# Performance work log

Hardware: AMD Instinct MI355X
Metric: run time of the kernel (lower is better)

The kernel has to match this reference:

```python
import jax, jax.numpy as jnp
import numpy as np


def setup_inputs() -> dict:
    key = jax.random.key(0)
    ks = jax.random.split(key, 8)
    B, T, U = 4, 256, 128
    De, Dp, D, V = 512, 512, 640, 1024
    s = lambda k, sh, fan: jax.random.normal(k, sh, dtype=jnp.float32) / np.sqrt(fan)
    return {
        "enc": jax.random.normal(ks[0], (B, T, De), dtype=jnp.float32),
        "pred": jax.random.normal(ks[1], (B, U, Dp), dtype=jnp.float32),
        "W_enc": s(ks[2], (De, D), De),
        "b_enc": jnp.zeros((D,), jnp.float32),
        "W_pred": s(ks[3], (Dp, D), Dp),
        "b_pred": jnp.zeros((D,), jnp.float32),
        "W_joint": s(ks[4], (D, V), D),
        "b_joint": jnp.zeros((V,), jnp.float32),
    }


def reference(enc, pred, W_enc, b_enc, W_pred, b_pred, W_joint, b_joint):
    # f: [B,T,D], g: [B,U,D]
    f = jnp.einsum("bte,ed->btd", enc, W_enc) + b_enc
    g = jnp.einsum("bup,pd->bud", pred, W_pred) + b_pred
    # broadcast-add over the T x U lattice, tanh activation
    joint = jnp.tanh(f[:, :, None, :] + g[:, None, :, :])  # [B,T,U,D]
    # final projection to num_classes
    out = jnp.einsum("btud,dv->btuv", joint, W_joint) + b_joint  # [B,T,U,V]
    return out
```

## Files before the change

### kernel.cpp

```cpp
#include <hip/hip_runtime.h>
#include <hip/hip_bf16.h>
#include <stdint.h>

typedef unsigned short u16;
typedef __attribute__((ext_vector_type(8))) __bf16 bf16x8;
typedef __attribute__((ext_vector_type(4))) float f32x4;
typedef __attribute__((ext_vector_type(8))) unsigned short u16x8;
typedef __attribute__((ext_vector_type(4))) unsigned int u32x4;

static __device__ __forceinline__ u16 f2bf(float x) {
  __hip_bfloat16 h = __float2bfloat16(x);
  u16 u;
  __builtin_memcpy(&u, &h, 2);
  return u;
}

static __device__ __forceinline__ float fast_tanh(float x) {
  float e = __expf(2.0f * x);
  return 1.0f - 2.0f * __builtin_amdgcn_rcpf(e + 1.0f);
}

static __device__ __forceinline__ void gload_lds16(const void* g, void* l) {
  __builtin_amdgcn_global_load_lds(
      (const __attribute__((address_space(1))) unsigned int*)g,
      (__attribute__((address_space(3))) unsigned int*)l, 16, 0, 0);
}

static __device__ __forceinline__ int swz(int row, int byte_in_row) {
  return row * 128 + (byte_in_row ^ ((row & 7) << 4));
}

__global__ __launch_bounds__(256) void transpose_cast_kernel(
    const float* __restrict__ in, u16* __restrict__ out, int K, int N) {
  int n = blockIdx.x;
  for (int k = threadIdx.x; k < K; k += 256) {
    out[(size_t)n * K + k] = f2bf(in[(size_t)k * N + n]);
  }
}

__global__ __launch_bounds__(256) void linear_kernel(
    const float* __restrict__ A, const u16* __restrict__ Wt,
    const float* __restrict__ bias, float* __restrict__ out) {
  __shared__ u16 sA[64 * 64];
  __shared__ u16 sB[64 * 64];
  const int t = threadIdx.x;
  const int bx = blockIdx.x;
  const int m0 = (bx / 10) * 64;
  const int n0 = (bx % 10) * 64;
  const int lane = t & 63, wid = t >> 6;
  const int wr = wid >> 1, wc = wid & 1;
  const int l15 = lane & 15, lk8 = (lane >> 4) << 3;

  const int srow = t >> 2;
  const int kc = (t & 3) << 4;

  f32x4 acc[2][2] = {};

  for (int k0 = 0; k0 < 512; k0 += 64) {
    {
      const float4* gp = (const float4*)(A + (size_t)(m0 + srow) * 512 + k0 + kc);
      u16 tmp[16];
#pragma unroll
      for (int i = 0; i < 4; ++i) {
        float4 v = gp[i];
        tmp[i * 4 + 0] = f2bf(v.x);
        tmp[i * 4 + 1] = f2bf(v.y);
        tmp[i * 4 + 2] = f2bf(v.z);
        tmp[i * 4 + 3] = f2bf(v.w);
      }
      *(u16x8*)((char*)sA + swz(srow, kc * 2)) = *(u16x8*)&tmp[0];
      *(u16x8*)((char*)sA + swz(srow, kc * 2 + 16)) = *(u16x8*)&tmp[8];
    }
    {
      const int off = (t & 3) << 5;
      const char* gsrc = (const char*)Wt + ((size_t)(n0 + srow) * 512 + k0) * 2 + off;
      u32x4 q0 = *(const u32x4*)gsrc;
      u32x4 q1 = *(const u32x4*)(gsrc + 16);
      *(u32x4*)((char*)sB + swz(srow, off)) = q0;
      *(u32x4*)((char*)sB + swz(srow, off + 16)) = q1;
    }
    __syncthreads();
#pragma unroll
    for (int kh = 0; kh < 2; ++kh) {
      const int kbyte = kh * 64 + lk8 * 2;
      bf16x8 av[2], bv[2];
#pragma unroll
      for (int mf = 0; mf < 2; ++mf)
        av[mf] = *(const bf16x8*)((char*)sA + swz(wr * 32 + mf * 16 + l15, kbyte));
#pragma unroll
      for (int nf = 0; nf < 2; ++nf)
        bv[nf] = *(const bf16x8*)((char*)sB + swz(wc * 32 + nf * 16 + l15, kbyte));
#pragma unroll
      for (int mf = 0; mf < 2; ++mf)
#pragma unroll
        for (int nf = 0; nf < 2; ++nf)
          acc[mf][nf] = __builtin_amdgcn_mfma_f32_16x16x32_bf16(
              av[mf], bv[nf], acc[mf][nf], 0, 0, 0);
    }
    __syncthreads();
  }

  const int r4 = (lane >> 4) << 2;
#pragma unroll
  for (int nf = 0; nf < 2; ++nf) {
    const int nc = n0 + wc * 32 + nf * 16 + l15;
    const float bjv = bias[nc];
#pragma unroll
    for (int mf = 0; mf < 2; ++mf) {
      const int mr = m0 + wr * 32 + mf * 16 + r4;
#pragma unroll
      for (int r = 0; r < 4; ++r)
        out[(size_t)(mr + r) * 640 + nc] = acc[mf][nf][r] + bjv;
    }
  }
}

__global__ __launch_bounds__(256) void joint_kernel(
    const float* __restrict__ f, const float* __restrict__ g,
    u16* __restrict__ joint, int m_base) {
  int idx = blockIdx.x * 256 + threadIdx.x;
  int row = idx / 80;
  int kc = (idx % 80) * 8;
  int m = m_base + row;
  int bt = m >> 7;
  int b = bt >> 8;
  int u = m & 127;
  const float4* fp = (const float4*)(f + (size_t)bt * 640 + kc);
  const float4* gp = (const float4*)(g + ((size_t)(b * 128 + u)) * 640 + kc);
  u16 tmp[8];
#pragma unroll
  for (int i = 0; i < 2; ++i) {
    float4 fv = fp[i];
    float4 gv = gp[i];
    tmp[i * 4 + 0] = f2bf(fast_tanh(fv.x + gv.x));
    tmp[i * 4 + 1] = f2bf(fast_tanh(fv.y + gv.y));
    tmp[i * 4 + 2] = f2bf(fast_tanh(fv.z + gv.z));
    tmp[i * 4 + 3] = f2bf(fast_tanh(fv.w + gv.w));
  }
  *(u16x8*)(joint + (size_t)row * 640 + kc) = *(u16x8*)&tmp[0];
}

__global__ __launch_bounds__(512, 2) void gemm256_kernel(
    const u16* __restrict__ A,
    const u16* __restrict__ Bt,
    const float* __restrict__ bias,
    float* __restrict__ out,
    int m_base, int mtiles) {
  extern __shared__ char smem[];
  const int t = threadIdx.x;
  const int lane = t & 63, wid = t >> 6;

  const int nwg = mtiles * 4;
  const int bid = blockIdx.x;
  const int q = nwg >> 3, r = nwg & 7;
  const int xcd = bid & 7, local = bid >> 3;
  const int wgid = (xcd < r ? xcd * (q + 1) : r * (q + 1) + (xcd - r) * q) + local;
  const int mt = wgid >> 2, nt = wgid & 3;

  const int wr = wid >> 2, wc = wid & 3;
  const int l15 = lane & 15;
  const int colbyte = (((lane >> 4) ^ ((l15 >> 1) & 3)) << 4);

  const int srow = lane >> 2;
  const int scol = ((lane & 3) ^ ((lane >> 3) & 3)) << 3;
  const u16* aS = A + (size_t)(mt * 256 + wid * 16 + srow) * 640 + scol;
  const u16* bS = Bt + (size_t)(nt * 256 + wid * 16 + srow) * 640 + scol;
  const int ldsbase = wid * 1024;

#define STAGE(kt, slot)                                              \
  do {                                                               \
    const int ko_ = (kt) * 32;                                       \
    char* sb_ = smem + (slot) * 32768;                               \
    gload_lds16(aS + ko_, sb_ + ldsbase);                            \
    gload_lds16(aS + 128 * 640 + ko_, sb_ + 8192 + ldsbase);         \
    gload_lds16(bS + ko_, sb_ + 16384 + ldsbase);                    \
    gload_lds16(bS + 128 * 640 + ko_, sb_ + 24576 + ldsbase);        \
  } while (0)

  f32x4 acc[8][4] = {};

  STAGE(0, 0);
  STAGE(1, 1);
  STAGE(2, 2);

  for (int tt = 0; tt < 20; ++tt) {
    asm volatile("s_waitcnt vmcnt(8)" ::: "memory");
    __builtin_amdgcn_s_barrier();
    __builtin_amdgcn_sched_barrier(0);
    const int kt = (tt + 3 > 19) ? 19 : tt + 3;
    STAGE(kt, (tt + 3) & 3);

    const char* sA = smem + (tt & 3) * 32768;
    const char* sB = sA + 16384;
    bf16x8 av[8], bv[4];
#pragma unroll
    for (int nf = 0; nf < 4; ++nf)
      bv[nf] = *(const bf16x8*)(sB + (wc * 64 + nf * 16 + l15) * 64 + colbyte);
#pragma unroll
    for (int mi = 0; mi < 8; ++mi)
      av[mi] = *(const bf16x8*)(sA + (wr * 128 + mi * 16 + l15) * 64 + colbyte);

    __builtin_amdgcn_s_setprio(1);
#pragma unroll
    for (int mi = 0; mi < 8; ++mi)
#pragma unroll
      for (int nf = 0; nf < 4; ++nf)
        acc[mi][nf] = __builtin_amdgcn_mfma_f32_16x16x32_bf16(
            av[mi], bv[nf], acc[mi][nf], 0, 0, 0);
    __builtin_amdgcn_s_setprio(0);
    __builtin_amdgcn_sched_barrier(0);
  }
#undef STAGE

  const int r4 = (lane >> 4) << 2;
#pragma unroll
  for (int nf = 0; nf < 4; ++nf) {
    const int v = nt * 256 + wc * 64 + nf * 16 + l15;
    const float bjv = bias[v];
#pragma unroll
    for (int mf = 0; mf < 8; ++mf) {
      const size_t m = (size_t)m_base + (size_t)mt * 256 + wr * 128 + mf * 16 + r4;
#pragma unroll
      for (int rr = 0; rr < 4; ++rr)
        out[(m + rr) * 1024 + v] = acc[mf][nf][rr] + bjv;
    }
  }
}

__global__ __launch_bounds__(512) void fused_joint_kernel(
    const float* __restrict__ f, const float* __restrict__ g,
    const u16* __restrict__ Wjt, const float* __restrict__ bj,
    float* __restrict__ out) {
  __shared__ u16 sA[128 * 64];
  __shared__ u16 sB[256 * 64];
  const int t = threadIdx.x;
  const int bt = blockIdx.x;
  const int b = bt >> 8;
  const int v0 = blockIdx.y << 8;
  const float* frow = f + (size_t)bt * 640;
  const float* gbase = g + (size_t)b * 128 * 640;

  const int lane = t & 63, wid = t >> 6;
  const int wr = wid >> 2, wc = wid & 3;
  const int l15 = lane & 15, lk8 = (lane >> 4) << 3;

  const int au = t >> 2;
  const int akc = (t & 3) << 4;
  const int bn = t >> 1;
  const int boff = (t & 1) << 6;

  f32x4 acc[4][4] = {};

  for (int k0 = 0; k0 < 640; k0 += 64) {
    {
      const float4* gp = (const float4*)(gbase + (size_t)au * 640 + k0 + akc);
      const float4* fp = (const float4*)(frow + k0 + akc);
      u16 tmp[16];
#pragma unroll
      for (int i = 0; i < 4; ++i) {
        float4 gv = gp[i];
        float4 fv = fp[i];
        tmp[i * 4 + 0] = f2bf(fast_tanh(gv.x + fv.x));
        tmp[i * 4 + 1] = f2bf(fast_tanh(gv.y + fv.y));
        tmp[i * 4 + 2] = f2bf(fast_tanh(gv.z + fv.z));
        tmp[i * 4 + 3] = f2bf(fast_tanh(gv.w + fv.w));
      }
      *(u16x8*)((char*)sA + swz(au, akc * 2)) = *(u16x8*)&tmp[0];
      *(u16x8*)((char*)sA + swz(au, akc * 2 + 16)) = *(u16x8*)&tmp[8];
    }
    {
      const char* gsrc = (const char*)Wjt + ((size_t)(v0 + bn) * 640 + k0) * 2 + boff;
#pragma unroll
      for (int i = 0; i < 4; ++i) {
        u32x4 qv = *(const u32x4*)(gsrc + i * 16);
        *(u32x4*)((char*)sB + swz(bn, boff + i * 16)) = qv;
      }
    }
    __syncthreads();
#pragma unroll
    for (int kh = 0; kh < 2; ++kh) {
      const int kbyte = kh * 64 + lk8 * 2;
      bf16x8 av[4], bv[4];
#pragma unroll
      for (int mf = 0; mf < 4; ++mf)
        av[mf] = *(const bf16x8*)((char*)sA + swz(wr * 64 + mf * 16 + l15, kbyte));
#pragma unroll
      for (int nf = 0; nf < 4; ++nf)
        bv[nf] = *(const bf16x8*)((char*)sB + swz(wc * 64 + nf * 16 + l15, kbyte));
#pragma unroll
      for (int mf = 0; mf < 4; ++mf)
#pragma unroll
        for (int nf = 0; nf < 4; ++nf)
          acc[mf][nf] = __builtin_amdgcn_mfma_f32_16x16x32_bf16(
              av[mf], bv[nf], acc[mf][nf], 0, 0, 0);
    }
    __syncthreads();
  }

  const int r4 = (lane >> 4) << 2;
#pragma unroll
  for (int nf = 0; nf < 4; ++nf) {
    const int v = v0 + wc * 64 + nf * 16 + l15;
    const float bjv = bj[v];
#pragma unroll
    for (int mf = 0; mf < 4; ++mf) {
      const int u = wr * 64 + mf * 16 + r4;
      const size_t o = ((size_t)bt * 128 + u) * 1024 + v;
#pragma unroll
      for (int rr = 0; rr < 4; ++rr)
        out[o + (size_t)rr * 1024] = acc[mf][nf][rr] + bjv;
    }
  }
}

extern "C" void kernel_launch(void* const* d_in, const int* in_sizes, int n_in,
                              void* d_out, int out_size, void* d_ws, size_t ws_size,
                              hipStream_t stream) {
  const float* enc = (const float*)d_in[0];
  const float* pred = (const float*)d_in[1];
  const float* W_enc = (const float*)d_in[2];
  const float* b_enc = (const float*)d_in[3];
  const float* W_pred = (const float*)d_in[4];
  const float* b_pred = (const float*)d_in[5];
  const float* W_joint = (const float*)d_in[6];
  const float* b_joint = (const float*)d_in[7];
  float* out = (float*)d_out;

  char* ws = (char*)d_ws;
  float* f = (float*)ws;
  float* gbuf = (float*)(ws + 2621440);
  u16* Wet = (u16*)(ws + 2621440 + 1310720);
  u16* Wpt = (u16*)(ws + 2621440 + 1310720 + 655360);
  u16* Wjt = (u16*)(ws + 2621440 + 1310720 + 2 * 655360);
  const size_t fixed = 2621440 + 1310720 + 2 * 655360 + 1310720;
  u16* joint = (u16*)(ws + fixed);

  transpose_cast_kernel<<<640, 256, 0, stream>>>(W_enc, Wet, 512, 640);
  transpose_cast_kernel<<<640, 256, 0, stream>>>(W_pred, Wpt, 512, 640);
  transpose_cast_kernel<<<1024, 256, 0, stream>>>(W_joint, Wjt, 640, 1024);

  linear_kernel<<<16 * 10, 256, 0, stream>>>(enc, Wet, b_enc, f);
  linear_kernel<<<8 * 10, 256, 0, stream>>>(pred, Wpt, b_pred, gbuf);

  const long TOTAL_M = 131072;
  long maxrows = ws_size > fixed ? (long)((ws_size - fixed) / 1280) : 0;
  maxrows &= ~255L;

  if (maxrows >= 16384) {
    (void)hipFuncSetAttribute((const void*)gemm256_kernel,
                              hipFuncAttributeMaxDynamicSharedMemorySize, 131072);
    long CH = maxrows >= TOTAL_M ? TOTAL_M : maxrows;
    for (long m0 = 0; m0 < TOTAL_M; m0 += CH) {
      long R = TOTAL_M - m0 < CH ? TOTAL_M - m0 : CH;
      int mtiles = (int)(R / 256);
      joint_kernel<<<(int)(R / 128) * 40, 256, 0, stream>>>(f, gbuf, joint, (int)m0);
      gemm256_kernel<<<mtiles * 4, 512, 131072, stream>>>(joint, Wjt, b_joint, out,
                                                          (int)m0, mtiles);
    }
  } else {
    fused_joint_kernel<<<dim3(1024, 4), 512, 0, stream>>>(f, gbuf, Wjt, b_joint, out);
  }
}
```

Before: 367.5 us.

## Restructure GEMM mainloop to double-buffered K=64 tiles with interleaved staging

Replaces the 4-slot K=32 pipeline in the projection GEMM with a 2-slot double buffer of K=64 tiles (128-byte LDS rows with a new XOR swizzle). Each iteration is split into four quarter phases that interleave LDS reads, MFMA bursts and the next tile's global-to-LDS loads. Each phase is separated by barriers and lgkmcnt waits. This halves the loop trip count and aims to overlap memory traffic with compute more finely. The cost is more barriers per iteration and a shallower prefetch distance, which could expose global load latency.

```diff
diff --git a/kernel.cpp b/kernel.cpp
--- a/kernel.cpp
+++ b/kernel.cpp
@@ -159,58 +159,101 @@
 
   const int wr = wid >> 2, wc = wid & 3;
   const int l15 = lane & 15;
-  const int colbyte = (((lane >> 4) ^ ((l15 >> 1) & 3)) << 4);
-
-  const int srow = lane >> 2;
-  const int scol = ((lane & 3) ^ ((lane >> 3) & 3)) << 3;
-  const u16* aS = A + (size_t)(mt * 256 + wid * 16 + srow) * 640 + scol;
-  const u16* bS = Bt + (size_t)(nt * 256 + wid * 16 + srow) * 640 + scol;
-  const int ldsbase = wid * 1024;
-
-#define STAGE(kt, slot)                                              \
-  do {                                                               \
-    const int ko_ = (kt) * 32;                                       \
-    char* sb_ = smem + (slot) * 32768;                               \
-    gload_lds16(aS + ko_, sb_ + ldsbase);                            \
-    gload_lds16(aS + 128 * 640 + ko_, sb_ + 8192 + ldsbase);         \
-    gload_lds16(bS + ko_, sb_ + 16384 + ldsbase);                    \
-    gload_lds16(bS + 128 * 640 + ko_, sb_ + 24576 + ldsbase);        \
+  const int kb16 = (lane >> 4) << 4;
+  const int rx = (l15 & 7) << 4;
+
+  const int scol = (((lane & 7) ^ (lane >> 3)) << 3);
+  const size_t rowsel = (size_t)(wid * 8 + (lane >> 3)) * 640 + scol;
+  const u16* a0 = A + (size_t)(mt * 256) * 640 + rowsel;
+  const u16* a1 = a0 + (size_t)64 * 640;
+  const u16* a2p = a0 + (size_t)128 * 640;
+  const u16* a3 = a0 + (size_t)192 * 640;
+  const u16* b0 = Bt + (size_t)(nt * 256) * 640 + rowsel;
+  const u16* b1 = b0 + (size_t)64 * 640;
+  const u16* b2p = b0 + (size_t)128 * 640;
+  const u16* b3 = b0 + (size_t)192 * 640;
+  const int ldst = wid * 1024;
+
+#define STAGE_HALF(kt, h, nb)                                               \
+  do {                                                                      \
+    const int ko_ = (kt) * 64;                                              \
+    gload_lds16(((h) == 0 ? a0 : (h) == 1 ? a2p : (h) == 2 ? b0 : b2p) + ko_, \
+                smem + (nb) + (h) * 16384 + ldst);                          \
+    gload_lds16(((h) == 0 ? a1 : (h) == 1 ? a3 : (h) == 2 ? b1 : b3) + ko_, \
+                smem + (nb) + (h) * 16384 + 8192 + ldst);                   \
   } while (0)
 
+#define DSREAD_B(kkb)                                                       \
+  _Pragma("unroll") for (int nf = 0; nf < 4; ++nf) bv[nf] =                 \
+      *(const bf16x8*)(sB + (wc * 64 + nf * 16 + l15) * 128 +               \
+                       (((kkb) + kb16) ^ rx));
+
+#define DSREAD_A(mi0, kkb)                                                  \
+  _Pragma("unroll") for (int i = 0; i < 4; ++i) av[i] =                     \
+      *(const bf16x8*)(sA + (wr * 128 + ((mi0) + i) * 16 + l15) * 128 +     \
+                       (((kkb) + kb16) ^ rx));
+
+#define MFMA16(mi0)                                                         \
+  __builtin_amdgcn_s_setprio(1);                                            \
+  _Pragma("unroll") for (int i = 0; i < 4; ++i)                             \
+  _Pragma("unroll") for (int nf = 0; nf < 4; ++nf)                          \
+      acc[(mi0) + i][nf] = __builtin_amdgcn_mfma_f32_16x16x32_bf16(         \
+          av[i], bv[nf], acc[(mi0) + i][nf], 0, 0, 0);                      \
+  __builtin_amdgcn_s_setprio(0);
+
+#define LGKM0()                                          \
+  asm volatile("s_waitcnt lgkmcnt(0)" ::: "memory");     \
+  __builtin_amdgcn_sched_barrier(0);
+
   f32x4 acc[8][4] = {};
 
-  STAGE(0, 0);
-  STAGE(1, 1);
-  STAGE(2, 2);
-
-  for (int tt = 0; tt < 20; ++tt) {
-    asm volatile("s_waitcnt vmcnt(8)" ::: "memory");
+  STAGE_HALF(0, 0, 0);
+  STAGE_HALF(0, 1, 0);
+  STAGE_HALF(0, 2, 0);
+  STAGE_HALF(0, 3, 0);
+
+  for (int tt = 0; tt < 10; ++tt) {
+    const int cur = (tt & 1) << 16;
+    const int nxt = cur ^ 65536;
+    const int kt = (tt + 1 < 10) ? tt + 1 : 9;
+    const char* sA = smem + cur;
+    const char* sB = smem + cur + 32768;
+    bf16x8 av[4], bv[4];
+
+    STAGE_HALF(kt, 0, nxt);
+    asm volatile("s_waitcnt vmcnt(2)" ::: "memory");
+    __builtin_amdgcn_sched_barrier(0);
     __builtin_amdgcn_s_barrier();
-    __builtin_amdgcn_sched_barrier(0);
-    const int kt = (tt + 3 > 19) ? 19 : tt + 3;
-    STAGE(kt, (tt + 3) & 3);
-
-    const char* sA = smem + (tt & 3) * 32768;
-    const char* sB = sA + 16384;
-    bf16x8 av[8], bv[4];
-#pragma unroll
-    for (int nf = 0; nf < 4; ++nf)
-      bv[nf] = *(const bf16x8*)(sB + (wc * 64 + nf * 16 + l15) * 64 + colbyte);
-#pragma unroll
-    for (int mi = 0; mi < 8; ++mi)
-      av[mi] = *(const bf16x8*)(sA + (wr * 128 + mi * 16 + l15) * 64 + colbyte);
-
-    __builtin_amdgcn_s_setprio(1);
-#pragma unroll
-    for (int mi = 0; mi < 8; ++mi)
-#pragma unroll
-      for (int nf = 0; nf < 4; ++nf)
-        acc[mi][nf] = __builtin_amdgcn_mfma_f32_16x16x32_bf16(
-            av[mi], bv[nf], acc[mi][nf], 0, 0, 0);
-    __builtin_amdgcn_s_setprio(0);
-    __builtin_amdgcn_sched_barrier(0);
-  }
-#undef STAGE
+    DSREAD_B(0)
+    DSREAD_A(0, 0)
+    LGKM0()
+    MFMA16(0)
+
+    DSREAD_A(4, 0)
+    STAGE_HALF(kt, 1, nxt);
+    __builtin_amdgcn_s_barrier();
+    LGKM0()
+    MFMA16(4)
+
+    DSREAD_B(64)
+    DSREAD_A(0, 64)
+    STAGE_HALF(kt, 2, nxt);
+    __builtin_amdgcn_s_barrier();
+    LGKM0()
+    MFMA16(0)
+
+    DSREAD_A(4, 64)
+    STAGE_HALF(kt, 3, nxt);
+    __builtin_amdgcn_s_barrier();
+    LGKM0()
+    MFMA16(4)
+    __builtin_amdgcn_s_barrier();
+  }
+#undef STAGE_HALF
+#undef DSREAD_B
+#undef DSREAD_A
+#undef MFMA16
+#undef LGKM0
 
   const int r4 = (lane >> 4) << 2;
 #pragma unroll
```

New measurement: 349.1 us. 5.0% less time.

## Load B fragments directly into registers and deepen K-tile for A via LDS

Applied to the files above, without the earlier changes.

The output GEMM now streams only the A (joint activations) tile through LDS, using 64-wide K tiles with an 8-way XOR swizzle. B (W_joint transposed) fragments are loaded from global memory straight into registers and double-buffered across iterations. The intent is to halve LDS traffic and barriers per K step and cut the loop trip count. The cost is more register pressure and B loads that bypass LDS and rely on cache hits. The hard-coded vmcnt waits also have to account for both load streams correctly.

```diff
diff --git a/kernel.cpp b/kernel.cpp
--- a/kernel.cpp
+++ b/kernel.cpp
@@ -159,58 +159,79 @@
 
   const int wr = wid >> 2, wc = wid & 3;
   const int l15 = lane & 15;
-  const int colbyte = (((lane >> 4) ^ ((l15 >> 1) & 3)) << 4);
-
-  const int srow = lane >> 2;
-  const int scol = ((lane & 3) ^ ((lane >> 3) & 3)) << 3;
-  const u16* aS = A + (size_t)(mt * 256 + wid * 16 + srow) * 640 + scol;
-  const u16* bS = Bt + (size_t)(nt * 256 + wid * 16 + srow) * 640 + scol;
-  const int ldsbase = wid * 1024;
-
-#define STAGE(kt, slot)                                              \
-  do {                                                               \
-    const int ko_ = (kt) * 32;                                       \
-    char* sb_ = smem + (slot) * 32768;                               \
-    gload_lds16(aS + ko_, sb_ + ldsbase);                            \
-    gload_lds16(aS + 128 * 640 + ko_, sb_ + 8192 + ldsbase);         \
-    gload_lds16(bS + ko_, sb_ + 16384 + ldsbase);                    \
-    gload_lds16(bS + 128 * 640 + ko_, sb_ + 24576 + ldsbase);        \
-  } while (0)
+  const int kb16 = (lane >> 4) << 4;
+  const int rx = (l15 & 7) << 4;
+
+  const int scol = (((lane & 7) ^ ((lane >> 3) & 7)) << 3);
+  const size_t rowsel = (size_t)(wid * 8 + (lane >> 3)) * 640 + scol;
+  const u16* aSrc[4];
+#pragma unroll
+  for (int j = 0; j < 4; ++j)
+    aSrc[j] = A + ((size_t)(mt * 256 + j * 64) * 640) + rowsel;
+  const int ldst = wid * 1024;
+
+  const u16* bG[4];
+#pragma unroll
+  for (int nf = 0; nf < 4; ++nf)
+    bG[nf] = Bt + (size_t)(nt * 256 + wc * 64 + nf * 16 + l15) * 640 +
+             ((lane >> 4) << 3);
 
   f32x4 acc[8][4] = {};
-
-  STAGE(0, 0);
-  STAGE(1, 1);
-  STAGE(2, 2);
-
-  for (int tt = 0; tt < 20; ++tt) {
-    asm volatile("s_waitcnt vmcnt(8)" ::: "memory");
-    __builtin_amdgcn_s_barrier();
-    __builtin_amdgcn_sched_barrier(0);
-    const int kt = (tt + 3 > 19) ? 19 : tt + 3;
-    STAGE(kt, (tt + 3) & 3);
-
-    const char* sA = smem + (tt & 3) * 32768;
-    const char* sB = sA + 16384;
-    bf16x8 av[8], bv[4];
-#pragma unroll
-    for (int nf = 0; nf < 4; ++nf)
-      bv[nf] = *(const bf16x8*)(sB + (wc * 64 + nf * 16 + l15) * 64 + colbyte);
-#pragma unroll
-    for (int mi = 0; mi < 8; ++mi)
-      av[mi] = *(const bf16x8*)(sA + (wr * 128 + mi * 16 + l15) * 64 + colbyte);
-
-    __builtin_amdgcn_s_setprio(1);
-#pragma unroll
-    for (int mi = 0; mi < 8; ++mi)
-#pragma unroll
-      for (int nf = 0; nf < 4; ++nf)
-        acc[mi][nf] = __builtin_amdgcn_mfma_f32_16x16x32_bf16(
-            av[mi], bv[nf], acc[mi][nf], 0, 0, 0);
-    __builtin_amdgcn_s_setprio(0);
-    __builtin_amdgcn_sched_barrier(0);
-  }
-#undef STAGE
+  bf16x8 bA[4][2], bB[4][2];
+
+#pragma unroll
+  for (int nf = 0; nf < 4; ++nf)
+#pragma unroll
+    for (int kk = 0; kk < 2; ++kk)
+      bA[nf][kk] = *(const bf16x8*)(bG[nf] + kk * 32);
+#pragma unroll
+  for (int j = 0; j < 4; ++j) {
+    gload_lds16(aSrc[j], smem + j * 8192 + ldst);
+    gload_lds16(aSrc[j] + 64, smem + 32768 + j * 8192 + ldst);
+    gload_lds16(aSrc[j] + 128, smem + 65536 + j * 8192 + ldst);
+  }
+
+#define GTILE(T, VM, BC, BN)                                                \
+  {                                                                         \
+    asm volatile("s_waitcnt vmcnt(" VM ")" ::: "memory");                   \
+    __builtin_amdgcn_s_barrier();                                           \
+    if ((T) < 9) {                                        \
+      _Pragma("unroll") for (int nf = 0; nf < 4; ++nf)                      \
+      _Pragma("unroll") for (int kk = 0; kk < 2; ++kk)                      \
+          BN[nf][kk] =                                                      \
+              *(const bf16x8*)(bG[nf] + ((T) + 1) * 64 + kk * 32);          \
+    }                                                                       \
+    if ((T) + 3 <= 9) {                 \
+      _Pragma("unroll") for (int j = 0; j < 4; ++j)                         \
+          gload_lds16(aSrc[j] + ((T) + 3) * 64,                             \
+                      smem + (((T) + 3) & 3) * 32768 + j * 8192 + ldst);    \
+    }                                                                       \
+    const char* sA_ = smem + ((T) & 3) * 32768;                             \
+    _Pragma("unroll") for (int kk = 0; kk < 2; ++kk) {                      \
+      bf16x8 av[8];                                                         \
+      _Pragma("unroll") for (int mi = 0; mi < 8; ++mi)                      \
+          av[mi] = *(const bf16x8*)(sA_ + (wr * 128 + mi * 16 + l15) * 128 +\
+                                    ((kk * 64 + kb16) ^ rx));               \
+      __builtin_amdgcn_s_setprio(1);                                        \
+      _Pragma("unroll") for (int mi = 0; mi < 8; ++mi)                      \
+      _Pragma("unroll") for (int nf = 0; nf < 4; ++nf)                      \
+          acc[mi][nf] = __builtin_amdgcn_mfma_f32_16x16x32_bf16(            \
+              av[mi], BC[nf][kk], acc[mi][nf], 0, 0, 0);                    \
+      __builtin_amdgcn_s_setprio(0);                                        \
+    }                                                                       \
+  }
+
+  GTILE(0, "0", bA, bB)
+  GTILE(1, "4", bB, bA)
+  GTILE(2, "4", bA, bB)
+  GTILE(3, "4", bB, bA)
+  GTILE(4, "4", bA, bB)
+  GTILE(5, "4", bB, bA)
+  GTILE(6, "4", bA, bB)
+  GTILE(7, "4", bB, bA)
+  GTILE(8, "0", bA, bB)
+  GTILE(9, "0", bB, bA)
+#undef GTILE
 
   const int r4 = (lane >> 4) << 2;
 #pragma unroll
```

After: 396.0 us. 7.7% more time.
